# Performance work log

Measured on AMD Instinct MI355X. Metric: run time of the kernel, lower is better.

The kernel has to match this reference:

```python
import jax, jax.numpy as jnp
import numpy as np

B, S, D = 4, 2048, 1024
E, H, TOP_K = 8, 4096, 2


def setup_inputs() -> dict:
    key = jax.random.key(0)
    ks = jax.random.split(key, 5)
    scale = 0.02
    return {
        "x": jax.random.normal(ks[0], (B, S, D), dtype=jnp.float32),
        "Wr": jax.random.normal(ks[1], (D, E), dtype=jnp.float32) * scale,
        "br": jnp.zeros((E,), dtype=jnp.float32),
        "W1": jax.random.normal(ks[2], (E, D, H), dtype=jnp.float32) * scale,
        "b1": jnp.zeros((E, H), dtype=jnp.float32),
        "W2": jax.random.normal(ks[3], (E, H, D), dtype=jnp.float32) * scale,
        "b2": jnp.zeros((E, D), dtype=jnp.float32),
    }


def reference(x, Wr, br, W1, b1, W2, b2):
    b, s, d = x.shape
    xf = x.reshape(-1, d)                                   # [T, D]
    gate = jax.nn.softmax(xf @ Wr + br, axis=-1)            # [T, E]
    top_w, top_i = jax.lax.top_k(gate, TOP_K)               # [T, K]
    top_w = top_w / jnp.sum(top_w, axis=-1, keepdims=True)
    # combine[t, e] = sum_i top_w[t, i] * 1{top_i[t, i] == e}
    combine = jnp.sum(jax.nn.one_hot(top_i, E, dtype=xf.dtype) * top_w[..., None], axis=1)  # [T, E]
    # Dense all-expert FFN (same math as the masked per-expert loops in torch)
    h = jax.nn.gelu(jnp.einsum('td,edh->teh', xf, W1) + b1, approximate=False)  # [T, E, H]
    out = jnp.einsum('teh,ehd,te->td', h, W2, combine) + combine @ b2           # [T, D]
    return out.reshape(b, s, d)
```

## Files before the change

### kernel.cpp

```cpp
#include <hip/hip_runtime.h>
#include <cstdio>


#define T_TOK 8192
#define DIM   1024
#define NEXP  8
#define HID   4096
#define MAXR  18432

typedef float          f32x4   __attribute__((ext_vector_type(4)));
typedef short          bf16x8  __attribute__((ext_vector_type(8)));
typedef unsigned short u16x4   __attribute__((ext_vector_type(4)));

static __device__ __forceinline__ unsigned short f2bf(float f) {
  unsigned int u = __builtin_bit_cast(unsigned int, f);
  u = (u + 0x7FFFu + ((u >> 16) & 1u)) >> 16;
  return (unsigned short)u;
}

static __device__ __forceinline__ void gl16(const void* g, void* l) {
  __builtin_amdgcn_global_load_lds(
      (const __attribute__((address_space(1))) unsigned int*)g,
      (__attribute__((address_space(3))) unsigned int*)l,
      16, 0, 0);
}

#define FENCE() asm volatile("" ::: "memory")

__global__ __launch_bounds__(256) void router_k(const float* __restrict__ x,
                                                const float* __restrict__ Wr,
                                                const float* __restrict__ br,
                                                int* __restrict__ meta,
                                                int2* __restrict__ top_i,
                                                float2* __restrict__ top_w) {
  int lane = threadIdx.x & 63;
  int wid  = threadIdx.x >> 6;
  int t = blockIdx.x * 4 + wid;
  const float* xp = x + (size_t)t * DIM + lane * 16;
  float acc[NEXP];
#pragma unroll
  for (int e = 0; e < NEXP; ++e) acc[e] = 0.f;
#pragma unroll
  for (int j = 0; j < 16; j += 4) {
    float4 xv = *(const float4*)(xp + j);
    const float* wp = Wr + (size_t)(lane * 16 + j) * NEXP;
#pragma unroll
    for (int jj = 0; jj < 4; ++jj) {
      float xs = jj == 0 ? xv.x : jj == 1 ? xv.y : jj == 2 ? xv.z : xv.w;
      float4 w0 = *(const float4*)(wp + jj * NEXP);
      float4 w1 = *(const float4*)(wp + jj * NEXP + 4);
      acc[0] += xs * w0.x; acc[1] += xs * w0.y; acc[2] += xs * w0.z; acc[3] += xs * w0.w;
      acc[4] += xs * w1.x; acc[5] += xs * w1.y; acc[6] += xs * w1.z; acc[7] += xs * w1.w;
    }
  }
#pragma unroll
  for (int off = 32; off > 0; off >>= 1) {
#pragma unroll
    for (int e = 0; e < NEXP; ++e) acc[e] += __shfl_xor(acc[e], off);
  }
  if (lane == 0) {
    float l[NEXP];
#pragma unroll
    for (int e = 0; e < NEXP; ++e) l[e] = acc[e] + br[e];
    int e1 = 0;
#pragma unroll
    for (int e = 1; e < NEXP; ++e) if (l[e] > l[e1]) e1 = e;
    int e2 = (e1 == 0) ? 1 : 0;
#pragma unroll
    for (int e = 0; e < NEXP; ++e) if (e != e1 && l[e] > l[e2]) e2 = e;
    float g  = expf(l[e2] - l[e1]);
    float w1 = 1.f / (1.f + g);
    top_i[t] = make_int2(e1, e2);
    top_w[t] = make_float2(w1, 1.f - w1);
    atomicAdd(&meta[e1], 1);
    atomicAdd(&meta[e2], 1);
  }
}

__global__ void prefix_k(int* __restrict__ meta) {
  if (threadIdx.x == 0) {
    int s = 0;
#pragma unroll
    for (int e = 0; e < NEXP; ++e) {
      meta[16 + e] = s;
      s += (meta[e] + 255) & ~255;
    }
    meta[24] = s;
    meta[25] = s;
  }
}

__global__ __launch_bounds__(256) void fill_k(int* __restrict__ tok_of_row,
                                              float* __restrict__ wt_of_row) {
  int i = blockIdx.x * 256 + threadIdx.x;
  if (i < MAXR) { tok_of_row[i] = 0; wt_of_row[i] = 0.f; }
}

__global__ __launch_bounds__(256) void scatter_k(const int2* __restrict__ top_i,
                                                 const float2* __restrict__ top_w,
                                                 int* __restrict__ meta,
                                                 int* __restrict__ row_of,
                                                 int* __restrict__ tok_of_row,
                                                 float* __restrict__ wt_of_row) {
  int t = blockIdx.x * 256 + threadIdx.x;
  int2  ei = top_i[t];
  float2 w = top_w[t];
  int p = atomicAdd(&meta[8 + ei.x], 1);
  int r = meta[16 + ei.x] + p;
  tok_of_row[r] = t; wt_of_row[r] = w.x; row_of[t * 2] = r;
  p = atomicAdd(&meta[8 + ei.y], 1);
  r = meta[16 + ei.y] + p;
  tok_of_row[r] = t; wt_of_row[r] = w.y; row_of[t * 2 + 1] = r;
}

__global__ __launch_bounds__(256) void gather_k(const float* __restrict__ x,
                                                const int* __restrict__ tok_of_row,
                                                const int* __restrict__ meta,
                                                unsigned short* __restrict__ xg) {
  int r = blockIdx.x;
  if (r >= meta[25]) return;
  int t = tok_of_row[r];
  int c = threadIdx.x * 4;
  float4 v = *(const float4*)(x + (size_t)t * DIM + c);
  u16x4 o;
  o[0] = f2bf(v.x); o[1] = f2bf(v.y); o[2] = f2bf(v.z); o[3] = f2bf(v.w);
  *(u16x4*)(xg + (size_t)r * DIM + c) = o;
}

__global__ __launch_bounds__(256) void transpose_convert_k(const float* __restrict__ W,
                                                           unsigned short* __restrict__ WT,
                                                           int R, int C) {
  __shared__ float tile[32][33];
  int e = blockIdx.z;
  int c0 = blockIdx.x * 32, r0 = blockIdx.y * 32;
  const float* Wp = W + (size_t)e * R * C;
  unsigned short* Op = WT + (size_t)e * R * C;
  int tr = threadIdx.x >> 3;
  int tc = (threadIdx.x & 7) * 4;
  float4 v = *(const float4*)(Wp + (size_t)(r0 + tr) * C + c0 + tc);
  tile[tr][tc] = v.x; tile[tr][tc + 1] = v.y; tile[tr][tc + 2] = v.z; tile[tr][tc + 3] = v.w;
  __syncthreads();
  int oc  = threadIdx.x >> 3;
  int orr = (threadIdx.x & 7) * 4;
  u16x4 o;
#pragma unroll
  for (int j = 0; j < 4; ++j) o[j] = f2bf(tile[orr + j][oc]);
  *(u16x4*)(Op + (size_t)(c0 + oc) * R + r0 + orr) = o;
}


template <int CUR, bool STG, bool LAST>
__device__ __forceinline__ void ktile(unsigned short* lds, int ko,
                                      const unsigned short* pA0, const unsigned short* pA1,
                                      const unsigned short* pB0, const unsigned short* pB1,
                                      int stL, int aoff, int boff, f32x4 (&acc)[4][4]) {
  constexpr int NXT = (CUR + 1) % 3;
  if constexpr (STG) {
    gl16(pA0 + ko, lds + NXT * 8192 + stL);
    gl16(pA1 + ko, lds + NXT * 8192 + stL + 2048);
    gl16(pB0 + ko, lds + NXT * 8192 + 4096 + stL);
    gl16(pB1 + ko, lds + NXT * 8192 + 4096 + stL + 2048);
    asm volatile("s_waitcnt vmcnt(4)" ::: "memory");
  } else {
    asm volatile("s_waitcnt vmcnt(0)" ::: "memory");
  }
  __builtin_amdgcn_s_barrier();
  FENCE();
  bf16x8 af[4], bv[4];
#pragma unroll
  for (int i = 0; i < 4; ++i)
    af[i] = *(const bf16x8*)(lds + CUR * 8192 + aoff + i * 512);
#pragma unroll
  for (int j = 0; j < 4; ++j)
    bv[j] = *(const bf16x8*)(lds + CUR * 8192 + boff + j * 512);
  __builtin_amdgcn_s_setprio(1);
#pragma unroll
  for (int i = 0; i < 4; ++i)
#pragma unroll
    for (int j = 0; j < 4; ++j)
      acc[i][j] = __builtin_amdgcn_mfma_f32_16x16x32_bf16(af[i], bv[j], acc[i][j], 0, 0, 0);
  __builtin_amdgcn_s_setprio(0);
  (void)ko;
}

template <int KTOT, int NTOT, int EPI>
__global__ __launch_bounds__(256, 3) void gemm3_k(const unsigned short* __restrict__ A,
                                                  const unsigned short* __restrict__ Bt,
                                                  const float* __restrict__ bias,
                                                  const int* __restrict__ meta,
                                                  const float* __restrict__ wt_of_row,
                                                  const int* __restrict__ tok_of_row,
                                                  void* __restrict__ Cout) {
  constexpr int NXB = MAXR / 128;
  constexpr int NWG = NXB * (NTOT / 128);
  constexpr int NKT = KTOT / 32;
  static_assert(NKT % 3 == 2, "tail handling assumes NKT % 3 == 2");
  __shared__ __align__(16) unsigned short lds[24576];

  int id = ((int)blockIdx.x & 7) * (NWG / 8) + ((int)blockIdx.x >> 3);
  int row0 = (id % NXB) * 128;
  int n0   = (id / NXB) * 128;
  if (row0 >= meta[25]) return;
  int e = 0;
  while (meta[17 + e] <= row0) ++e;
  const unsigned short* Bp = Bt + (size_t)e * NTOT * KTOT;

  int tid = threadIdx.x;
  int lane = tid & 63, wid = tid >> 6;
  int wm = wid >> 1, wn = wid & 1;

  int s = (tid & 3) ^ ((tid >> 3) & 3);
  const unsigned short* pA0 = A + (size_t)(row0 + (tid >> 2)) * KTOT + s * 8;
  const unsigned short* pA1 = pA0 + (size_t)64 * KTOT;
  const unsigned short* pB0 = Bp + (size_t)(n0 + (tid >> 2)) * KTOT + s * 8;
  const unsigned short* pB1 = pB0 + (size_t)64 * KTOT;
  int stL = wid * 512;

  int am = lane & 15;
  int sF = ((lane >> 4) ^ ((lane >> 1) & 3)) * 8;
  int aoff = (wm * 64 + am) * 32 + sF;
  int boff = 4096 + (wn * 64 + am) * 32 + sF;

  f32x4 acc[4][4];
#pragma unroll
  for (int i = 0; i < 4; ++i)
#pragma unroll
    for (int j = 0; j < 4; ++j) acc[i][j] = (f32x4){0.f, 0.f, 0.f, 0.f};

  gl16(pA0, lds + stL);          gl16(pA1, lds + stL + 2048);
  gl16(pB0, lds + 4096 + stL);   gl16(pB1, lds + 4096 + stL + 2048);
  FENCE();

  for (int t = 0; t < NKT - 2; t += 3) {
    ktile<0, true, false>(lds, (t + 1) * 32, pA0, pA1, pB0, pB1, stL, aoff, boff, acc);
    ktile<1, true, false>(lds, (t + 2) * 32, pA0, pA1, pB0, pB1, stL, aoff, boff, acc);
    ktile<2, true, false>(lds, (t + 3) * 32, pA0, pA1, pB0, pB1, stL, aoff, boff, acc);
  }
  ktile<0, true, false>(lds, (NKT - 1) * 32, pA0, pA1, pB0, pB1, stL, aoff, boff, acc);
  ktile<1, false, true>(lds, 0, pA0, pA1, pB0, pB1, stL, aoff, boff, acc);

  int rbase = row0 + wm * 64 + ((lane >> 4) << 2);
  int nbase = n0 + wn * 64 + am;
  if constexpr (EPI == 0) {
    unsigned short* Hp = (unsigned short*)Cout;
    const float* bp = bias + (size_t)e * NTOT;
#pragma unroll
    for (int i = 0; i < 4; ++i)
#pragma unroll
      for (int j = 0; j < 4; ++j) {
        int n = nbase + j * 16;
        float bv = bp[n];
#pragma unroll
        for (int g = 0; g < 4; ++g) {
          int m = rbase + i * 16 + g;
          float v = acc[i][j][g] + bv;
          v = 0.5f * v * (1.f + erff(v * 0.70710678118654752f));
          Hp[(size_t)m * NTOT + n] = f2bf(v);
        }
      }
  } else {
    float* Op = (float*)Cout;
    const float* bp = bias + (size_t)e * NTOT;
#pragma unroll
    for (int i = 0; i < 4; ++i)
#pragma unroll
      for (int g = 0; g < 4; ++g) {
        int m = rbase + i * 16 + g;
        float wt = wt_of_row[m];
        if (wt != 0.f) {
          float* orow = Op + (size_t)tok_of_row[m] * DIM;
#pragma unroll
          for (int j = 0; j < 4; ++j) {
            int n = nbase + j * 16;
            atomicAdd(orow + n, (acc[i][j][g] + bp[n]) * wt);
          }
        }
      }
  }
}

extern "C" void kernel_launch(void* const* d_in, const int* in_sizes, int n_in,
                              void* d_out, int out_size, void* d_ws, size_t ws_size,
                              hipStream_t stream) {
  const float* x  = (const float*)d_in[0];
  const float* Wr = (const float*)d_in[1];
  const float* br = (const float*)d_in[2];
  const float* W1 = (const float*)d_in[3];
  const float* b1 = (const float*)d_in[4];
  const float* W2 = (const float*)d_in[5];
  const float* b2 = (const float*)d_in[6];
  float* out = (float*)d_out;

  char* base = (char*)d_ws;
  size_t off = 0;
  auto carve = [&](size_t bytes) -> void* {
    void* r = base + off;
    off = (off + bytes + 255) & ~(size_t)255;
    return r;
  };
  int*            meta       = (int*)carve(26 * 4);
  int2*           top_i      = (int2*)carve((size_t)T_TOK * 8);
  float2*         top_w      = (float2*)carve((size_t)T_TOK * 8);
  int*            row_of     = (int*)carve((size_t)T_TOK * 2 * 4);
  int*            tok_of_row = (int*)carve((size_t)MAXR * 4);
  float*          wt_of_row  = (float*)carve((size_t)MAXR * 4);
  unsigned short* xg         = (unsigned short*)carve((size_t)MAXR * DIM * 2);
  unsigned short* W1bT       = (unsigned short*)carve((size_t)NEXP * DIM * HID * 2);
  unsigned short* W2bT       = (unsigned short*)carve((size_t)NEXP * DIM * HID * 2);
  unsigned short* hbuf       = (unsigned short*)carve((size_t)MAXR * HID * 2);
  if (off > ws_size) {
    fprintf(stderr, "kernel_launch: ws_size too small: need %zu have %zu\n", off, ws_size);
    return;
  }

  hipMemsetAsync(meta, 0, 26 * 4, stream);
  hipMemsetAsync(out, 0, (size_t)out_size * 4, stream);
  hipLaunchKernelGGL(transpose_convert_k, dim3(HID / 32, DIM / 32, NEXP), dim3(256), 0, stream,
                     W1, W1bT, DIM, HID);
  hipLaunchKernelGGL(transpose_convert_k, dim3(DIM / 32, HID / 32, NEXP), dim3(256), 0, stream,
                     W2, W2bT, HID, DIM);
  hipLaunchKernelGGL(fill_k, dim3((MAXR + 255) / 256), dim3(256), 0, stream,
                     tok_of_row, wt_of_row);
  hipLaunchKernelGGL(router_k, dim3(T_TOK / 4), dim3(256), 0, stream,
                     x, Wr, br, meta, top_i, top_w);
  hipLaunchKernelGGL(prefix_k, dim3(1), dim3(64), 0, stream, meta);
  hipLaunchKernelGGL(scatter_k, dim3(T_TOK / 256), dim3(256), 0, stream,
                     top_i, top_w, meta, row_of, tok_of_row, wt_of_row);
  hipLaunchKernelGGL(gather_k, dim3(MAXR), dim3(256), 0, stream, x, tok_of_row, meta, xg);
  hipLaunchKernelGGL((gemm3_k<DIM, HID, 0>), dim3((MAXR / 128) * (HID / 128)), dim3(256), 0,
                     stream, xg, W1bT, b1, meta, wt_of_row, tok_of_row, (void*)hbuf);
  hipLaunchKernelGGL((gemm3_k<HID, DIM, 1>), dim3((MAXR / 128) * (DIM / 128)), dim3(256), 0,
                     stream, hbuf, W2bT, b2, meta, wt_of_row, tok_of_row, (void*)out);
}
```

Measured before the change: 924.9 us.

## Fuse prep kernels and replace triple-buffered GEMM with single-buffer high-occupancy loop

New measurement: 2.422 ms. 2.62x slower.

```diff
diff --git a/kernel.cpp b/kernel.cpp
--- a/kernel.cpp
+++ b/kernel.cpp
@@ -25,17 +25,35 @@
       16, 0, 0);
 }
 
-#define FENCE() asm volatile("" ::: "memory")
-
-__global__ __launch_bounds__(256) void router_k(const float* __restrict__ x,
-                                                const float* __restrict__ Wr,
-                                                const float* __restrict__ br,
-                                                int* __restrict__ meta,
-                                                int2* __restrict__ top_i,
-                                                float2* __restrict__ top_w) {
+static __device__ __forceinline__ void transpose_body(const float* __restrict__ W,
+                                                      unsigned short* __restrict__ WT,
+                                                      int R, int C, int bx, int by, int e,
+                                                      float (*tile)[33]) {
+  int c0 = bx * 32, r0 = by * 32;
+  const float* Wp = W + (size_t)e * R * C;
+  unsigned short* Op = WT + (size_t)e * R * C;
+  int tr = threadIdx.x >> 3;
+  int tc = (threadIdx.x & 7) * 4;
+  float4 v = *(const float4*)(Wp + (size_t)(r0 + tr) * C + c0 + tc);
+  tile[tr][tc] = v.x; tile[tr][tc + 1] = v.y; tile[tr][tc + 2] = v.z; tile[tr][tc + 3] = v.w;
+  __syncthreads();
+  int oc  = threadIdx.x >> 3;
+  int orr = (threadIdx.x & 7) * 4;
+  u16x4 o;
+#pragma unroll
+  for (int j = 0; j < 4; ++j) o[j] = f2bf(tile[orr + j][oc]);
+  *(u16x4*)(Op + (size_t)(c0 + oc) * R + r0 + orr) = o;
+}
+
+static __device__ __forceinline__ void router_body(int blk, const float* __restrict__ x,
+                                                   const float* __restrict__ Wr,
+                                                   const float* __restrict__ br,
+                                                   int* __restrict__ meta,
+                                                   int2* __restrict__ top_i,
+                                                   float2* __restrict__ top_w) {
   int lane = threadIdx.x & 63;
   int wid  = threadIdx.x >> 6;
-  int t = blockIdx.x * 4 + wid;
+  int t = blk * 4 + wid;
   const float* xp = x + (size_t)t * DIM + lane * 16;
   float acc[NEXP];
 #pragma unroll
@@ -77,6 +95,33 @@
   }
 }
 
+__global__ __launch_bounds__(256) void prep_k(const float* __restrict__ W1,
+                                              const float* __restrict__ W2,
+                                              unsigned short* __restrict__ W1bT,
+                                              unsigned short* __restrict__ W2bT,
+                                              const float* __restrict__ x,
+                                              const float* __restrict__ Wr,
+                                              const float* __restrict__ br,
+                                              int* __restrict__ meta,
+                                              int2* __restrict__ top_i,
+                                              float2* __restrict__ top_w,
+                                              int* __restrict__ tok_of_row,
+                                              float* __restrict__ wt_of_row) {
+  __shared__ float tile[32][33];
+  int id = blockIdx.x;
+  if (id < 32768) {
+    transpose_body(W1, W1bT, DIM, HID, id & 127, (id >> 7) & 31, id >> 12, tile);
+  } else if (id < 65536) {
+    int id2 = id - 32768;
+    transpose_body(W2, W2bT, HID, DIM, id2 & 31, (id2 >> 5) & 127, id2 >> 12, tile);
+  } else if (id < 67584) {
+    router_body(id - 65536, x, Wr, br, meta, top_i, top_w);
+  } else {
+    int i = (id - 67584) * 256 + threadIdx.x;
+    if (i < MAXR) { tok_of_row[i] = 0; wt_of_row[i] = 0.f; }
+  }
+}
+
 __global__ void prefix_k(int* __restrict__ meta) {
   if (threadIdx.x == 0) {
     int s = 0;
@@ -88,12 +133,6 @@
     meta[24] = s;
     meta[25] = s;
   }
-}
-
-__global__ __launch_bounds__(256) void fill_k(int* __restrict__ tok_of_row,
-                                              float* __restrict__ wt_of_row) {
-  int i = blockIdx.x * 256 + threadIdx.x;
-  if (i < MAXR) { tok_of_row[i] = 0; wt_of_row[i] = 0.f; }
 }
 
 __global__ __launch_bounds__(256) void scatter_k(const int2* __restrict__ top_i,
@@ -127,79 +166,24 @@
   *(u16x4*)(xg + (size_t)r * DIM + c) = o;
 }
 
-__global__ __launch_bounds__(256) void transpose_convert_k(const float* __restrict__ W,
-                                                           unsigned short* __restrict__ WT,
-                                                           int R, int C) {
-  __shared__ float tile[32][33];
-  int e = blockIdx.z;
-  int c0 = blockIdx.x * 32, r0 = blockIdx.y * 32;
-  const float* Wp = W + (size_t)e * R * C;
-  unsigned short* Op = WT + (size_t)e * R * C;
-  int tr = threadIdx.x >> 3;
-  int tc = (threadIdx.x & 7) * 4;
-  float4 v = *(const float4*)(Wp + (size_t)(r0 + tr) * C + c0 + tc);
-  tile[tr][tc] = v.x; tile[tr][tc + 1] = v.y; tile[tr][tc + 2] = v.z; tile[tr][tc + 3] = v.w;
-  __syncthreads();
-  int oc  = threadIdx.x >> 3;
-  int orr = (threadIdx.x & 7) * 4;
-  u16x4 o;
-#pragma unroll
-  for (int j = 0; j < 4; ++j) o[j] = f2bf(tile[orr + j][oc]);
-  *(u16x4*)(Op + (size_t)(c0 + oc) * R + r0 + orr) = o;
-}
-
-
-template <int CUR, bool STG, bool LAST>
-__device__ __forceinline__ void ktile(unsigned short* lds, int ko,
-                                      const unsigned short* pA0, const unsigned short* pA1,
-                                      const unsigned short* pB0, const unsigned short* pB1,
-                                      int stL, int aoff, int boff, f32x4 (&acc)[4][4]) {
-  constexpr int NXT = (CUR + 1) % 3;
-  if constexpr (STG) {
-    gl16(pA0 + ko, lds + NXT * 8192 + stL);
-    gl16(pA1 + ko, lds + NXT * 8192 + stL + 2048);
-    gl16(pB0 + ko, lds + NXT * 8192 + 4096 + stL);
-    gl16(pB1 + ko, lds + NXT * 8192 + 4096 + stL + 2048);
-    asm volatile("s_waitcnt vmcnt(4)" ::: "memory");
-  } else {
-    asm volatile("s_waitcnt vmcnt(0)" ::: "memory");
-  }
-  __builtin_amdgcn_s_barrier();
-  FENCE();
-  bf16x8 af[4], bv[4];
-#pragma unroll
-  for (int i = 0; i < 4; ++i)
-    af[i] = *(const bf16x8*)(lds + CUR * 8192 + aoff + i * 512);
-#pragma unroll
-  for (int j = 0; j < 4; ++j)
-    bv[j] = *(const bf16x8*)(lds + CUR * 8192 + boff + j * 512);
-  __builtin_amdgcn_s_setprio(1);
-#pragma unroll
-  for (int i = 0; i < 4; ++i)
-#pragma unroll
-    for (int j = 0; j < 4; ++j)
-      acc[i][j] = __builtin_amdgcn_mfma_f32_16x16x32_bf16(af[i], bv[j], acc[i][j], 0, 0, 0);
-  __builtin_amdgcn_s_setprio(0);
-  (void)ko;
-}
 
 template <int KTOT, int NTOT, int EPI>
-__global__ __launch_bounds__(256, 3) void gemm3_k(const unsigned short* __restrict__ A,
-                                                  const unsigned short* __restrict__ Bt,
-                                                  const float* __restrict__ bias,
-                                                  const int* __restrict__ meta,
-                                                  const float* __restrict__ wt_of_row,
-                                                  const int* __restrict__ tok_of_row,
-                                                  void* __restrict__ Cout) {
+__global__ __launch_bounds__(256, 6) void gemmv7_k(const unsigned short* __restrict__ A,
+                                                   const unsigned short* __restrict__ Bt,
+                                                   const float* __restrict__ bias,
+                                                   const int* __restrict__ meta,
+                                                   const float* __restrict__ wt_of_row,
+                                                   const int* __restrict__ tok_of_row,
+                                                   void* __restrict__ Cout) {
+  constexpr int NN  = NTOT / 128;
   constexpr int NXB = MAXR / 128;
-  constexpr int NWG = NXB * (NTOT / 128);
+  constexpr int NWG = NXB * NN;
   constexpr int NKT = KTOT / 32;
-  static_assert(NKT % 3 == 2, "tail handling assumes NKT % 3 == 2");
-  __shared__ __align__(16) unsigned short lds[24576];
+  __shared__ __align__(16) unsigned short lds[8192];
 
   int id = ((int)blockIdx.x & 7) * (NWG / 8) + ((int)blockIdx.x >> 3);
-  int row0 = (id % NXB) * 128;
-  int n0   = (id / NXB) * 128;
+  int n0   = (id % NN) * 128;
+  int row0 = (id / NN) * 128;
   if (row0 >= meta[25]) return;
   int e = 0;
   while (meta[17 + e] <= row0) ++e;
@@ -214,7 +198,6 @@
   const unsigned short* pA1 = pA0 + (size_t)64 * KTOT;
   const unsigned short* pB0 = Bp + (size_t)(n0 + (tid >> 2)) * KTOT + s * 8;
   const unsigned short* pB1 = pB0 + (size_t)64 * KTOT;
-  int stL = wid * 512;
 
   int am = lane & 15;
   int sF = ((lane >> 4) ^ ((lane >> 1) & 3)) * 8;
@@ -227,17 +210,26 @@
 #pragma unroll
     for (int j = 0; j < 4; ++j) acc[i][j] = (f32x4){0.f, 0.f, 0.f, 0.f};
 
-  gl16(pA0, lds + stL);          gl16(pA1, lds + stL + 2048);
-  gl16(pB0, lds + 4096 + stL);   gl16(pB1, lds + 4096 + stL + 2048);
-  FENCE();
-
-  for (int t = 0; t < NKT - 2; t += 3) {
-    ktile<0, true, false>(lds, (t + 1) * 32, pA0, pA1, pB0, pB1, stL, aoff, boff, acc);
-    ktile<1, true, false>(lds, (t + 2) * 32, pA0, pA1, pB0, pB1, stL, aoff, boff, acc);
-    ktile<2, true, false>(lds, (t + 3) * 32, pA0, pA1, pB0, pB1, stL, aoff, boff, acc);
-  }
-  ktile<0, true, false>(lds, (NKT - 1) * 32, pA0, pA1, pB0, pB1, stL, aoff, boff, acc);
-  ktile<1, false, true>(lds, 0, pA0, pA1, pB0, pB1, stL, aoff, boff, acc);
+  for (int kt = 0; kt < NKT; ++kt) {
+    __syncthreads();
+    gl16(pA0 + kt * 32, lds + tid * 8);
+    gl16(pA1 + kt * 32, lds + 2048 + tid * 8);
+    gl16(pB0 + kt * 32, lds + 4096 + tid * 8);
+    gl16(pB1 + kt * 32, lds + 6144 + tid * 8);
+    __syncthreads();
+    bf16x8 af[4], bv[4];
+#pragma unroll
+    for (int i = 0; i < 4; ++i)
+      af[i] = *(const bf16x8*)(lds + aoff + i * 512);
+#pragma unroll
+    for (int j = 0; j < 4; ++j)
+      bv[j] = *(const bf16x8*)(lds + boff + j * 512);
+#pragma unroll
+    for (int i = 0; i < 4; ++i)
+#pragma unroll
+      for (int j = 0; j < 4; ++j)
+        acc[i][j] = __builtin_amdgcn_mfma_f32_16x16x32_bf16(af[i], bv[j], acc[i][j], 0, 0, 0);
+  }
 
   int rbase = row0 + wm * 64 + ((lane >> 4) << 2);
   int nbase = n0 + wn * 64 + am;
@@ -255,7 +247,7 @@
           int m = rbase + i * 16 + g;
           float v = acc[i][j][g] + bv;
           v = 0.5f * v * (1.f + erff(v * 0.70710678118654752f));
-          Hp[(size_t)m * NTOT + n] = f2bf(v);
+          __builtin_nontemporal_store(f2bf(v), Hp + (size_t)m * NTOT + n);
         }
       }
   } else {
@@ -315,20 +307,15 @@
 
   hipMemsetAsync(meta, 0, 26 * 4, stream);
   hipMemsetAsync(out, 0, (size_t)out_size * 4, stream);
-  hipLaunchKernelGGL(transpose_convert_k, dim3(HID / 32, DIM / 32, NEXP), dim3(256), 0, stream,
-                     W1, W1bT, DIM, HID);
-  hipLaunchKernelGGL(transpose_convert_k, dim3(DIM / 32, HID / 32, NEXP), dim3(256), 0, stream,
-                     W2, W2bT, HID, DIM);
-  hipLaunchKernelGGL(fill_k, dim3((MAXR + 255) / 256), dim3(256), 0, stream,
+  hipLaunchKernelGGL(prep_k, dim3(67656), dim3(256), 0, stream,
+                     W1, W2, W1bT, W2bT, x, Wr, br, meta, top_i, top_w,
                      tok_of_row, wt_of_row);
-  hipLaunchKernelGGL(router_k, dim3(T_TOK / 4), dim3(256), 0, stream,
-                     x, Wr, br, meta, top_i, top_w);
   hipLaunchKernelGGL(prefix_k, dim3(1), dim3(64), 0, stream, meta);
   hipLaunchKernelGGL(scatter_k, dim3(T_TOK / 256), dim3(256), 0, stream,
                      top_i, top_w, meta, row_of, tok_of_row, wt_of_row);
   hipLaunchKernelGGL(gather_k, dim3(MAXR), dim3(256), 0, stream, x, tok_of_row, meta, xg);
-  hipLaunchKernelGGL((gemm3_k<DIM, HID, 0>), dim3((MAXR / 128) * (HID / 128)), dim3(256), 0,
+  hipLaunchKernelGGL((gemmv7_k<DIM, HID, 0>), dim3((MAXR / 128) * (HID / 128)), dim3(256), 0,
                      stream, xg, W1bT, b1, meta, wt_of_row, tok_of_row, (void*)hbuf);
-  hipLaunchKernelGGL((gemm3_k<HID, DIM, 1>), dim3((MAXR / 128) * (DIM / 128)), dim3(256), 0,
+  hipLaunchKernelGGL((gemmv7_k<HID, DIM, 1>), dim3((MAXR / 128) * (DIM / 128)), dim3(256), 0,
                      stream, hbuf, W2bT, b2, meta, wt_of_row, tok_of_row, (void*)out);
 }
```
